# Performance work log

Measured on AMD Instinct MI355X. Metric: run time of the kernel, lower is better.

## Reference

```python
import jax, jax.numpy as jnp
import numpy as np

B, N, D = 2, 2048, 1024
RANK, HEADS = 256, 16
HS = RANK // HEADS          # 16, low-rank head size for QK
DH = D // HEADS             # 64, value head size
SCALE = 1.0 / np.sqrt(HS)


def setup_inputs() -> dict:
    key = jax.random.key(0)
    k1, k2, k3 = jax.random.split(key, 3)
    x = jax.random.normal(k1, (B, N, D), dtype=jnp.float32)
    # causal additive mask, 0 on/below diag, -1e9 above
    mask = jnp.where(jnp.tril(jnp.ones((N, N), dtype=bool)), 0.0, -1e9).astype(jnp.float32)
    Wqk = jax.random.normal(k2, (2 * RANK, D), dtype=jnp.float32) * (1.0 / np.sqrt(D))
    Wv = jax.random.normal(k3, (D, D), dtype=jnp.float32) * (1.0 / np.sqrt(D))
    return {"x": x, "mask": mask, "Wqk": Wqk, "Wv": Wv}


def reference(x, mask, Wqk, Wv):
    b, n, d = x.shape
    qk = jnp.einsum('bnd,rd->bnr', x, Wqk)            # [b,n,2*rank]
    q, k = jnp.split(qk, 2, axis=-1)                  # [b,n,rank] each
    # L2 normalize over FULL rank dim (before head split), clamp norm >= 1e-6
    q = q / jnp.maximum(jnp.linalg.norm(q, axis=-1, keepdims=True), 1e-6)
    k = k / jnp.maximum(jnp.linalg.norm(k, axis=-1, keepdims=True), 1e-6)
    q = q.reshape(b, n, HEADS, HS).transpose(0, 2, 1, 3)   # [b,h,n,hs]
    k = k.reshape(b, n, HEADS, HS).transpose(0, 2, 1, 3)
    v = jnp.einsum('bnd,ed->bne', x, Wv).reshape(b, n, HEADS, DH).transpose(0, 2, 1, 3)  # [b,h,n,dh]
    att = jnp.einsum('bhqe,bhke->bhqk', q, k) * SCALE
    att = jnp.clip(att, -10000.0, 10000.0)
    att = att + mask[None, None, :, :]
    att = jax.nn.softmax(att, axis=-1)
    # NaN guard: zero NaNs then renormalize (no-op when no NaNs)
    att = jnp.where(jnp.isnan(att), 0.0, att)
    att = att / jnp.maximum(att.sum(axis=-1, keepdims=True), 1e-6)
    y = jnp.einsum('bhqk,bhkd->bhqd', att, v)              # [b,h,n,dh]
    return y.transpose(0, 2, 1, 3).reshape(b, n, d)
```

## Files before the change

kernel.cpp:

```cpp
#include <hip/hip_runtime.h>
#include <math.h>

#define BATCH 2
#define SEQ   2048
#define DIM   1024
#define RANK  256
#define HEADS 16
#define HS    16
#define DH    64
#define MROWS 4096

#define QSCALE 0.36067376f

typedef __attribute__((ext_vector_type(8)))  short    short8;
typedef __attribute__((ext_vector_type(4)))  float    f32x4;
typedef __attribute__((ext_vector_type(16))) float    f32x16;
typedef __attribute__((ext_vector_type(2)))  unsigned uint2v;

#define GPTR const __attribute__((address_space(1))) unsigned int*
#define LPTR __attribute__((address_space(3))) unsigned int*

__device__ __forceinline__ unsigned short f2bf(float f) {
    union { float f; unsigned u; } v; v.f = f;
    return (unsigned short)((v.u + 0x7FFFu + ((v.u >> 16) & 1u)) >> 16);
}
__device__ __forceinline__ float bf2f(unsigned short h) {
    union { unsigned u; float f; } v; v.u = ((unsigned)h) << 16;
    return v.f;
}

#define XQ   1048576
#define WQKQ 131072
#define WVQ  262144
__global__ __launch_bounds__(256) void conv3(const float* __restrict__ x,
                                             const float* __restrict__ wqk,
                                             const float* __restrict__ wv,
                                             unsigned short* __restrict__ xb,
                                             unsigned short* __restrict__ wcat)
{
    const int i = blockIdx.x * 256 + threadIdx.x;
    const float* src; unsigned short* dst; int j;
    if (i < XQ)              { src = x;   dst = xb;   j = i; }
    else if (i < XQ + WQKQ)  { src = wqk; dst = wcat; j = i - XQ; }
    else                     { src = wv;  dst = wcat + (size_t)4 * WQKQ; j = i - XQ - WQKQ; }
    float4 v = ((const float4*)src)[j];
    ushort4 o; o.x = f2bf(v.x); o.y = f2bf(v.y); o.z = f2bf(v.z); o.w = f2bf(v.w);
    ((ushort4*)dst)[j] = o;
}

__global__ __launch_bounds__(256, 3) void gemm_mfma(const unsigned short* __restrict__ A,
                                                    const unsigned short* __restrict__ W,
                                                    unsigned short* __restrict__ qkb,
                                                    unsigned short* __restrict__ vt)
{
    __shared__ __align__(16) unsigned short Alds[2][128 * 64];
    __shared__ __align__(16) unsigned short Blds[2][64 * 64];

    const int tid = threadIdx.x;
    const int w = tid >> 6, lane = tid & 63;
    const int lr = lane & 15, lg = lane >> 4;
    const int wm = w >> 1, wn = w & 1;

    const int Lf = blockIdx.x;
    const int xcd = Lf & 7;
    const int i5 = Lf >> 3;
    const int bm = (4 * xcd + (i5 & 3)) * 128;
    const int bn = (i5 >> 2) * 64;

    const int rs = lane >> 3, cs = lane & 7;

    f32x4 acc[4][2] = {};

#define STAGEG(kt_, buf_) do {                                                        \
        const int k0_ = (kt_) * 64;                                                   \
        _Pragma("unroll")                                                             \
        for (int i = 0; i < 4; ++i) {                                                 \
            const int r = w * 32 + i * 8 + rs;                                        \
            __builtin_amdgcn_global_load_lds(                                         \
                (GPTR)&A[(size_t)(bm + r) * 1024 + k0_ + 8 * (cs ^ (r & 7))],         \
                (LPTR)&Alds[buf_][(w * 32 + i * 8) * 64], 16, 0, 0);                  \
        }                                                                             \
        _Pragma("unroll")                                                             \
        for (int i = 0; i < 2; ++i) {                                                 \
            const int r = w * 16 + i * 8 + rs;                                        \
            __builtin_amdgcn_global_load_lds(                                         \
                (GPTR)&W[(size_t)(bn + r) * 1024 + k0_ + 8 * (cs ^ (r & 7))],         \
                (LPTR)&Blds[buf_][(w * 16 + i * 8) * 64], 16, 0, 0);                  \
        }                                                                             \
    } while (0)

    STAGEG(0, 0);

    #pragma unroll 1
    for (int kt = 0; kt < 16; ++kt) {
        if (kt + 1 < 16) {
            STAGEG(kt + 1, (kt + 1) & 1);
            asm volatile("s_waitcnt vmcnt(6)" ::: "memory");
        } else {
            asm volatile("s_waitcnt vmcnt(0)" ::: "memory");
        }
        __builtin_amdgcn_sched_barrier(0);
        __builtin_amdgcn_s_barrier();

        const int buf = kt & 1;
        #pragma unroll
        for (int kk = 0; kk < 2; ++kk) {
            short8 af[4], bfr[2];
            #pragma unroll
            for (int mi = 0; mi < 4; ++mi) {
                const int row = wm * 64 + mi * 16 + lr;
                af[mi] = *(const short8*)&Alds[buf][row * 64 + 8 * ((kk * 4 + lg) ^ (row & 7))];
            }
            #pragma unroll
            for (int ni = 0; ni < 2; ++ni) {
                const int row = wn * 32 + ni * 16 + lr;
                bfr[ni] = *(const short8*)&Blds[buf][row * 64 + 8 * ((kk * 4 + lg) ^ (row & 7))];
            }
            #pragma unroll
            for (int mi = 0; mi < 4; ++mi)
                #pragma unroll
                for (int ni = 0; ni < 2; ++ni)
                    acc[mi][ni] = __builtin_amdgcn_mfma_f32_16x16x32_bf16(af[mi], bfr[ni], acc[mi][ni], 0, 0, 0);
        }
        __builtin_amdgcn_s_barrier();
    }
#undef STAGEG

    if (bn < 512) {
        #pragma unroll
        for (int mi = 0; mi < 4; ++mi) {
            const int rbase = bm + wm * 64 + mi * 16 + lg * 4;
            #pragma unroll
            for (int ni = 0; ni < 2; ++ni) {
                const int col = bn + wn * 32 + ni * 16 + lr;
                #pragma unroll
                for (int r = 0; r < 4; ++r)
                    qkb[(size_t)(rbase + r) * 512 + col] = f2bf(acc[mi][ni][r]);
            }
        }
    } else {
        const int nb = bn - 512;
        #pragma unroll
        for (int mi = 0; mi < 4; ++mi) {
            const int m = bm + wm * 64 + mi * 16 + lg * 4;
            const int bb = m >> 11, ms = m & 2047;
            #pragma unroll
            for (int ni = 0; ni < 2; ++ni) {
                const int d = nb + wn * 32 + ni * 16 + lr;
                ushort4 pk;
                pk.x = f2bf(acc[mi][ni][0]); pk.y = f2bf(acc[mi][ni][1]);
                pk.z = f2bf(acc[mi][ni][2]); pk.w = f2bf(acc[mi][ni][3]);
                *(ushort4*)&vt[((size_t)bb * DIM + d) * SEQ + ms] = pk;
            }
        }
    }
}

__global__ __launch_bounds__(256) void l2norm_split(const unsigned short* __restrict__ qkb,
                                                    unsigned short* __restrict__ qn,
                                                    unsigned short* __restrict__ kn)
{
    const int row = blockIdx.x;
    const int t = threadIdx.x;
    const unsigned short* p = qkb + (size_t)row * 512;
    float q = bf2f(p[t]);
    float k = bf2f(p[t + 256]);
    float sq = q * q, sk = k * k;
    #pragma unroll
    for (int off = 32; off > 0; off >>= 1) {
        sq += __shfl_down(sq, off);
        sk += __shfl_down(sk, off);
    }
    __shared__ float sh[8];
    const int wid = t >> 6;
    if ((t & 63) == 0) { sh[wid * 2] = sq; sh[wid * 2 + 1] = sk; }
    __syncthreads();
    sq = sh[0] + sh[2] + sh[4] + sh[6];
    sk = sh[1] + sh[3] + sh[5] + sh[7];
    const float rq = QSCALE / fmaxf(sqrtf(sq), 1e-6f);
    const float rk = 1.0f   / fmaxf(sqrtf(sk), 1e-6f);

    const int b = row >> 11, n = row & 2047;
    const int head = t >> 4, hs = t & 15;
    const size_t o = (((size_t)b * HEADS + head) * SEQ + n) * 16 + hs;
    qn[o] = f2bf(q * rq);
    kn[o] = f2bf(k * rk);
}

template<bool MASK>
__device__ __forceinline__ void segpv(const short8 ak0, const short8 ak1, const short8 bq,
                                      const unsigned short* Vs, int kb, int kh, int hi,
                                      int l31, int qg, f32x16 o[2], float& lp)
{
    const f32x16 z = {};
    short8 pa[4];

    const f32x16 s0 = __builtin_amdgcn_mfma_f32_32x32x16_bf16(ak0, bq, z, 0, 0, 0);
    {
        float p0[16];
        #pragma unroll
        for (int r = 0; r < 16; ++r) {
            float e = __builtin_exp2f(s0[r]);
            if (MASK) {
                const int kl = kb + (r & 3) + 8 * (r >> 2) + 4 * hi;
                e = (kl > qg) ? 0.0f : e;
            }
            p0[r] = e; lp += e;
        }
        #pragma unroll
        for (int g = 0; g < 2; ++g) {
            const int jj = 2 * g;
            unsigned a0, a1, b0, b1;
            asm("v_cvt_pk_bf16_f32 %0, %1, %2" : "=v"(a0) : "v"(p0[4*jj]),     "v"(p0[4*jj + 1]));
            asm("v_cvt_pk_bf16_f32 %0, %1, %2" : "=v"(b0) : "v"(p0[4*jj + 2]), "v"(p0[4*jj + 3]));
            asm("v_cvt_pk_bf16_f32 %0, %1, %2" : "=v"(a1) : "v"(p0[4*jj + 4]), "v"(p0[4*jj + 5]));
            asm("v_cvt_pk_bf16_f32 %0, %1, %2" : "=v"(b1) : "v"(p0[4*jj + 6]), "v"(p0[4*jj + 7]));
            const uint2v r0 = __builtin_amdgcn_permlane32_swap(a0, a1, false, false);
            const uint2v r1 = __builtin_amdgcn_permlane32_swap(b0, b1, false, false);
            union { short8 s; unsigned u[4]; } pu;
            pu.u[0] = r0[0]; pu.u[1] = r1[0]; pu.u[2] = r0[1]; pu.u[3] = r1[1];
            pa[g] = pu.s;
        }
    }
    const f32x16 s1 = __builtin_amdgcn_mfma_f32_32x32x16_bf16(ak1, bq, z, 0, 0, 0);
    {
        float p1[16];
        #pragma unroll
        for (int r = 0; r < 16; ++r) {
            float e = __builtin_exp2f(s1[r]);
            if (MASK) {
                const int kl = kb + 32 + (r & 3) + 8 * (r >> 2) + 4 * hi;
                e = (kl > qg) ? 0.0f : e;
            }
            p1[r] = e; lp += e;
        }
        #pragma unroll
        for (int g = 0; g < 2; ++g) {
            const int jj = 2 * g;
            unsigned a0, a1, b0, b1;
            asm("v_cvt_pk_bf16_f32 %0, %1, %2" : "=v"(a0) : "v"(p1[4*jj]),     "v"(p1[4*jj + 1]));
            asm("v_cvt_pk_bf16_f32 %0, %1, %2" : "=v"(b0) : "v"(p1[4*jj + 2]), "v"(p1[4*jj + 3]));
            asm("v_cvt_pk_bf16_f32 %0, %1, %2" : "=v"(a1) : "v"(p1[4*jj + 4]), "v"(p1[4*jj + 5]));
            asm("v_cvt_pk_bf16_f32 %0, %1, %2" : "=v"(b1) : "v"(p1[4*jj + 6]), "v"(p1[4*jj + 7]));
            const uint2v r0 = __builtin_amdgcn_permlane32_swap(a0, a1, false, false);
            const uint2v r1 = __builtin_amdgcn_permlane32_swap(b0, b1, false, false);
            union { short8 s; unsigned u[4]; } pu;
            pu.u[0] = r0[0]; pu.u[1] = r1[0]; pu.u[2] = r0[1]; pu.u[3] = r1[1];
            pa[2 + g] = pu.s;
        }
    }

    #pragma unroll
    for (int g = 0; g < 4; ++g)
        #pragma unroll
        for (int half = 0; half < 2; ++half) {
            const int row = half * 32 + l31;
            const int slot = (8 * kh + 2 * g + hi) ^ (row & 15);
            const short8 bv = *(const short8*)&Vs[row * 128 + 8 * slot];
            o[half] = __builtin_amdgcn_mfma_f32_32x32x16_bf16(pa[g], bv, o[half], 0, 0, 0);
        }
}

__global__ __launch_bounds__(512, 4) void attn_w8(const unsigned short* __restrict__ qn,
                                                  const unsigned short* __restrict__ kn,
                                                  const unsigned short* __restrict__ vt,
                                                  float* __restrict__ out)
{
    const int L = blockIdx.x;
    const int bh = L & 31;
    const int p  = L >> 5;
    const int h = bh & 15, b = bh >> 4;

    const int tid = threadIdx.x, w = tid >> 6, lane = tid & 63;
    const int seg = w >> 2, qh = (w >> 1) & 1, kh = w & 1;
    const int l31 = lane & 31, hi = lane >> 5;

    const int qt  = seg ? p : 31 - p;
    const int nts = (qt >> 1) + 1;
    const int nt0 = ((31 - p) >> 1) + 1;
    const int band = qt * 64 + qh * 32;
    const int qg = band + l31;

    __shared__ __align__(16) unsigned char smem[33792];

    const unsigned short* qbh = qn + (size_t)bh * SEQ * 16;
    const unsigned short* kbh = kn + (size_t)bh * SEQ * 16;

    const short8 bq = *(const short8*)&qbh[qg * 16 + 8 * hi];

    f32x16 o[2] = {};
    float lp = 0.0f;

    const unsigned short* kwin = kbh + (64 * kh + l31) * 16 + 8 * hi;
    short8 ak0 = *(const short8*)(kwin);
    short8 ak1 = *(const short8*)(kwin + 32 * 16);

    const int vsub = lane >> 4, vslot = lane & 15;

#define STAGEV(kt_, buf_) do {                                                                    \
        const int k0_ = (kt_) * 128;                                                              \
        _Pragma("unroll")                                                                         \
        for (int i = 0; i < 2; ++i) {                                                             \
            const int c = 2 * w + i;                                                              \
            const int dh = 4 * c + vsub;                                                          \
            const int so = 8 * (vslot ^ (dh & 15));                                               \
            __builtin_amdgcn_global_load_lds(                                                     \
                (GPTR)&vt[((size_t)b * DIM + h * DH + dh) * SEQ + k0_ + so],                      \
                (LPTR)(smem + (buf_) * 16384 + c * 1024), 16, 0, 0);                              \
        }                                                                                         \
    } while (0)

    STAGEV(0, 0);

    #pragma unroll 1
    for (int kt = 0; kt < nt0; ++kt) {
        short8 an0 = ak0, an1 = ak1;
        if (kt + 1 < nt0) {
            STAGEV(kt + 1, (kt + 1) & 1);
            an0 = *(const short8*)(kwin + (size_t)(kt + 1) * 128 * 16);
            an1 = *(const short8*)(kwin + (size_t)(kt + 1) * 128 * 16 + 32 * 16);
            asm volatile("s_waitcnt vmcnt(4)" ::: "memory");
        } else {
            asm volatile("s_waitcnt vmcnt(0)" ::: "memory");
        }
        __builtin_amdgcn_sched_barrier(0);
        __builtin_amdgcn_s_barrier();

        if (kt < nts) {
            const unsigned short* Vs = (const unsigned short*)(smem + (kt & 1) * 16384);
            const int kb = kt * 128 + 64 * kh;
            __builtin_amdgcn_s_setprio(1);
            if (kt < nts - 1) {
                segpv<false>(ak0, ak1, bq, Vs, kb, kh, hi, l31, qg, o, lp);
            } else if (kb <= band + 31) {
                if (kb + 63 <= band) segpv<false>(ak0, ak1, bq, Vs, kb, kh, hi, l31, qg, o, lp);
                else                 segpv<true >(ak0, ak1, bq, Vs, kb, kh, hi, l31, qg, o, lp);
            }
            __builtin_amdgcn_s_setprio(0);
        }

        ak0 = an0; ak1 = an1;
        __builtin_amdgcn_s_barrier();
    }
#undef STAGEV

    lp += __shfl_xor(lp, 32);

    __syncthreads();
    float* Os = (float*)(smem + seg * 16384);
    float* Ls = (float*)(smem + 32768 + seg * 512);

    if (kh == 1) {
        #pragma unroll
        for (int half = 0; half < 2; ++half)
            #pragma unroll
            for (int r = 0; r < 16; ++r) {
                const int q = (r & 3) + 8 * (r >> 2) + 4 * hi;
                Os[(qh * 32 + q) * 64 + half * 32 + l31] = o[half][r];
            }
        Ls[qh * 64 + lane] = lp;
    }
    __syncthreads();
    if (kh == 0) {
        const float lt = lp + Ls[qh * 64 + lane];
        const float inv = 1.0f / fmaxf(lt, 1e-6f);
        #pragma unroll
        for (int r = 0; r < 16; ++r) {
            const int q = (r & 3) + 8 * (r >> 2) + 4 * hi;
            const float iv = __shfl(inv, q);
            #pragma unroll
            for (int half = 0; half < 2; ++half) {
                const float v = (o[half][r] + Os[(qh * 32 + q) * 64 + half * 32 + l31]) * iv;
                __builtin_nontemporal_store(v,
                    &out[((size_t)b * SEQ + band + q) * DIM + h * DH + half * 32 + l31]);
            }
        }
    }
}

extern "C" void kernel_launch(void* const* d_in, const int* in_sizes, int n_in,
                              void* d_out, int out_size, void* d_ws, size_t ws_size,
                              hipStream_t stream)
{
    const float* x   = (const float*)d_in[0];
    const float* Wqk = (const float*)d_in[2];
    const float* Wv  = (const float*)d_in[3];
    float* out = (float*)d_out;

    unsigned short* xb   = (unsigned short*)d_ws;
    unsigned short* qkb  = xb  + (size_t)MROWS * DIM;
    unsigned short* vt   = qkb + (size_t)MROWS * 512;
    unsigned short* wcat = vt  + (size_t)BATCH * DIM * SEQ;
    unsigned short* qn = xb;
    unsigned short* kn = xb + (size_t)32 * SEQ * 16;

    conv3<<<5632, 256, 0, stream>>>(x, Wqk, Wv, xb, wcat);
    gemm_mfma<<<768, 256, 0, stream>>>(xb, wcat, qkb, vt);
    l2norm_split<<<MROWS, 256, 0, stream>>>(qkb, qn, kn);
    attn_w8<<<512, 512, 0, stream>>>(qn, kn, vt, out);
}
```

Measured before the change: 67.37 us.

## Process both query halves per wave reusing V fragments; polynomial exp2

```diff
diff --git a/kernel.cpp b/kernel.cpp
--- a/kernel.cpp
+++ b/kernel.cpp
@@ -27,6 +27,10 @@
 __device__ __forceinline__ float bf2f(unsigned short h) {
     union { unsigned u; float f; } v; v.u = ((unsigned)h) << 16;
     return v.f;
+}
+
+__device__ __forceinline__ float exp2_poly(float x) {
+    return fmaf(x, fmaf(x, fmaf(x, 0.05550411f, 0.24022651f), 0.69314718f), 1.0f);
 }
 
 #define XQ   1048576
@@ -187,84 +191,72 @@
     kn[o] = f2bf(k * rk);
 }
 
+
 template<bool MASK>
-__device__ __forceinline__ void segpv(const short8 ak0, const short8 ak1, const short8 bq,
-                                      const unsigned short* Vs, int kb, int kh, int hi,
-                                      int l31, int qg, f32x16 o[2], float& lp)
+__device__ __forceinline__ void qpv(const short8 ak0, const short8 ak1, const short8 bq,
+                                    const short8 vb[4][2], int kb, int hi, int qg,
+                                    f32x16 o[2], float& lp)
 {
     const f32x16 z = {};
     short8 pa[4];
 
     const f32x16 s0 = __builtin_amdgcn_mfma_f32_32x32x16_bf16(ak0, bq, z, 0, 0, 0);
-    {
-        float p0[16];
-        #pragma unroll
-        for (int r = 0; r < 16; ++r) {
-            float e = __builtin_exp2f(s0[r]);
-            if (MASK) {
-                const int kl = kb + (r & 3) + 8 * (r >> 2) + 4 * hi;
-                e = (kl > qg) ? 0.0f : e;
-            }
-            p0[r] = e; lp += e;
-        }
-        #pragma unroll
-        for (int g = 0; g < 2; ++g) {
-            const int jj = 2 * g;
-            unsigned a0, a1, b0, b1;
-            asm("v_cvt_pk_bf16_f32 %0, %1, %2" : "=v"(a0) : "v"(p0[4*jj]),     "v"(p0[4*jj + 1]));
-            asm("v_cvt_pk_bf16_f32 %0, %1, %2" : "=v"(b0) : "v"(p0[4*jj + 2]), "v"(p0[4*jj + 3]));
-            asm("v_cvt_pk_bf16_f32 %0, %1, %2" : "=v"(a1) : "v"(p0[4*jj + 4]), "v"(p0[4*jj + 5]));
-            asm("v_cvt_pk_bf16_f32 %0, %1, %2" : "=v"(b1) : "v"(p0[4*jj + 6]), "v"(p0[4*jj + 7]));
-            const uint2v r0 = __builtin_amdgcn_permlane32_swap(a0, a1, false, false);
-            const uint2v r1 = __builtin_amdgcn_permlane32_swap(b0, b1, false, false);
-            union { short8 s; unsigned u[4]; } pu;
-            pu.u[0] = r0[0]; pu.u[1] = r1[0]; pu.u[2] = r0[1]; pu.u[3] = r1[1];
-            pa[g] = pu.s;
-        }
-    }
     const f32x16 s1 = __builtin_amdgcn_mfma_f32_32x32x16_bf16(ak1, bq, z, 0, 0, 0);
-    {
-        float p1[16];
-        #pragma unroll
-        for (int r = 0; r < 16; ++r) {
-            float e = __builtin_exp2f(s1[r]);
-            if (MASK) {
-                const int kl = kb + 32 + (r & 3) + 8 * (r >> 2) + 4 * hi;
-                e = (kl > qg) ? 0.0f : e;
-            }
-            p1[r] = e; lp += e;
-        }
-        #pragma unroll
-        for (int g = 0; g < 2; ++g) {
-            const int jj = 2 * g;
-            unsigned a0, a1, b0, b1;
-            asm("v_cvt_pk_bf16_f32 %0, %1, %2" : "=v"(a0) : "v"(p1[4*jj]),     "v"(p1[4*jj + 1]));
-            asm("v_cvt_pk_bf16_f32 %0, %1, %2" : "=v"(b0) : "v"(p1[4*jj + 2]), "v"(p1[4*jj + 3]));
-            asm("v_cvt_pk_bf16_f32 %0, %1, %2" : "=v"(a1) : "v"(p1[4*jj + 4]), "v"(p1[4*jj + 5]));
-            asm("v_cvt_pk_bf16_f32 %0, %1, %2" : "=v"(b1) : "v"(p1[4*jj + 6]), "v"(p1[4*jj + 7]));
-            const uint2v r0 = __builtin_amdgcn_permlane32_swap(a0, a1, false, false);
-            const uint2v r1 = __builtin_amdgcn_permlane32_swap(b0, b1, false, false);
-            union { short8 s; unsigned u[4]; } pu;
-            pu.u[0] = r0[0]; pu.u[1] = r1[0]; pu.u[2] = r0[1]; pu.u[3] = r1[1];
-            pa[2 + g] = pu.s;
-        }
+
+    float p0[16], p1[16];
+    #pragma unroll
+    for (int r = 0; r < 16; ++r) {
+        float e0 = exp2_poly(s0[r]);
+        float e1 = exp2_poly(s1[r]);
+        if (MASK) {
+            const int kl = kb + (r & 3) + 8 * (r >> 2) + 4 * hi;
+            e0 = (kl > qg) ? 0.0f : e0;
+            e1 = (kl + 32 > qg) ? 0.0f : e1;
+        }
+        p0[r] = e0; p1[r] = e1;
+        lp += e0 + e1;
+    }
+
+    #pragma unroll
+    for (int g = 0; g < 4; ++g) {
+        const float* pc = (g < 2) ? p0 : p1;
+        const int jj = 2 * (g & 1);
+        unsigned a0, a1, b0, b1;
+        asm("v_cvt_pk_bf16_f32 %0, %1, %2" : "=v"(a0) : "v"(pc[4*jj]),     "v"(pc[4*jj + 1]));
+        asm("v_cvt_pk_bf16_f32 %0, %1, %2" : "=v"(b0) : "v"(pc[4*jj + 2]), "v"(pc[4*jj + 3]));
+        asm("v_cvt_pk_bf16_f32 %0, %1, %2" : "=v"(a1) : "v"(pc[4*jj + 4]), "v"(pc[4*jj + 5]));
+        asm("v_cvt_pk_bf16_f32 %0, %1, %2" : "=v"(b1) : "v"(pc[4*jj + 6]), "v"(pc[4*jj + 7]));
+        const uint2v r0 = __builtin_amdgcn_permlane32_swap(a0, a1, false, false);
+        const uint2v r1 = __builtin_amdgcn_permlane32_swap(b0, b1, false, false);
+        union { short8 s; unsigned u[4]; } pu;
+        pu.u[0] = r0[0]; pu.u[1] = r1[0]; pu.u[2] = r0[1]; pu.u[3] = r1[1];
+        pa[g] = pu.s;
     }
 
     #pragma unroll
     for (int g = 0; g < 4; ++g)
         #pragma unroll
-        for (int half = 0; half < 2; ++half) {
-            const int row = half * 32 + l31;
-            const int slot = (8 * kh + 2 * g + hi) ^ (row & 15);
-            const short8 bv = *(const short8*)&Vs[row * 128 + 8 * slot];
-            o[half] = __builtin_amdgcn_mfma_f32_32x32x16_bf16(pa[g], bv, o[half], 0, 0, 0);
-        }
-}
-
-__global__ __launch_bounds__(512, 4) void attn_w8(const unsigned short* __restrict__ qn,
-                                                  const unsigned short* __restrict__ kn,
-                                                  const unsigned short* __restrict__ vt,
-                                                  float* __restrict__ out)
+        for (int half = 0; half < 2; ++half)
+            o[half] = __builtin_amdgcn_mfma_f32_32x32x16_bf16(pa[g], vb[g][half], o[half], 0, 0, 0);
+}
+
+__device__ __forceinline__ void qdisp(bool last, const short8 ak0, const short8 ak1,
+                                      const short8 bq, const short8 vb[4][2], int kb,
+                                      int hi, int qmin, int qg,
+                                      f32x16 o[2], float& lp)
+{
+    if (!last) {
+        qpv<false>(ak0, ak1, bq, vb, kb, hi, qg, o, lp);
+    } else if (kb <= qmin + 31) {
+        if (kb + 63 <= qmin) qpv<false>(ak0, ak1, bq, vb, kb, hi, qg, o, lp);
+        else                 qpv<true >(ak0, ak1, bq, vb, kb, hi, qg, o, lp);
+    }
+}
+
+__global__ __launch_bounds__(256, 2) void attn_q64(const unsigned short* __restrict__ qn,
+                                                   const unsigned short* __restrict__ kn,
+                                                   const unsigned short* __restrict__ vt,
+                                                   float* __restrict__ out)
 {
     const int L = blockIdx.x;
     const int bh = L & 31;
@@ -272,24 +264,25 @@
     const int h = bh & 15, b = bh >> 4;
 
     const int tid = threadIdx.x, w = tid >> 6, lane = tid & 63;
-    const int seg = w >> 2, qh = (w >> 1) & 1, kh = w & 1;
+    const int seg = w >> 1, kh = w & 1;
     const int l31 = lane & 31, hi = lane >> 5;
 
     const int qt  = seg ? p : 31 - p;
     const int nts = (qt >> 1) + 1;
     const int nt0 = ((31 - p) >> 1) + 1;
-    const int band = qt * 64 + qh * 32;
-    const int qg = band + l31;
+    const int qmin0 = qt * 64, qmin1 = qt * 64 + 32;
+    const int qg0 = qmin0 + l31, qg1 = qmin1 + l31;
 
     __shared__ __align__(16) unsigned char smem[33792];
 
     const unsigned short* qbh = qn + (size_t)bh * SEQ * 16;
     const unsigned short* kbh = kn + (size_t)bh * SEQ * 16;
 
-    const short8 bq = *(const short8*)&qbh[qg * 16 + 8 * hi];
-
-    f32x16 o[2] = {};
-    float lp = 0.0f;
+    const short8 bq0 = *(const short8*)&qbh[qg0 * 16 + 8 * hi];
+    const short8 bq1 = *(const short8*)&qbh[qg1 * 16 + 8 * hi];
+
+    f32x16 o0[2] = {}, o1[2] = {};
+    float lp0 = 0.0f, lp1 = 0.0f;
 
     const unsigned short* kwin = kbh + (64 * kh + l31) * 16 + 8 * hi;
     short8 ak0 = *(const short8*)(kwin);
@@ -300,8 +293,8 @@
 #define STAGEV(kt_, buf_) do {                                                                    \
         const int k0_ = (kt_) * 128;                                                              \
         _Pragma("unroll")                                                                         \
-        for (int i = 0; i < 2; ++i) {                                                             \
-            const int c = 2 * w + i;                                                              \
+        for (int i = 0; i < 4; ++i) {                                                             \
+            const int c = 4 * w + i;                                                              \
             const int dh = 4 * c + vsub;                                                          \
             const int so = 8 * (vslot ^ (dh & 15));                                               \
             __builtin_amdgcn_global_load_lds(                                                     \
@@ -319,7 +312,7 @@
             STAGEV(kt + 1, (kt + 1) & 1);
             an0 = *(const short8*)(kwin + (size_t)(kt + 1) * 128 * 16);
             an1 = *(const short8*)(kwin + (size_t)(kt + 1) * 128 * 16 + 32 * 16);
-            asm volatile("s_waitcnt vmcnt(4)" ::: "memory");
+            asm volatile("s_waitcnt vmcnt(6)" ::: "memory");
         } else {
             asm volatile("s_waitcnt vmcnt(0)" ::: "memory");
         }
@@ -329,13 +322,21 @@
         if (kt < nts) {
             const unsigned short* Vs = (const unsigned short*)(smem + (kt & 1) * 16384);
             const int kb = kt * 128 + 64 * kh;
+
+            short8 vb[4][2];
+            #pragma unroll
+            for (int g = 0; g < 4; ++g)
+                #pragma unroll
+                for (int half = 0; half < 2; ++half) {
+                    const int row = half * 32 + l31;
+                    const int slot = (8 * kh + 2 * g + hi) ^ (row & 15);
+                    vb[g][half] = *(const short8*)&Vs[row * 128 + 8 * slot];
+                }
+
+            const bool last = (kt == nts - 1);
             __builtin_amdgcn_s_setprio(1);
-            if (kt < nts - 1) {
-                segpv<false>(ak0, ak1, bq, Vs, kb, kh, hi, l31, qg, o, lp);
-            } else if (kb <= band + 31) {
-                if (kb + 63 <= band) segpv<false>(ak0, ak1, bq, Vs, kb, kh, hi, l31, qg, o, lp);
-                else                 segpv<true >(ak0, ak1, bq, Vs, kb, kh, hi, l31, qg, o, lp);
-            }
+            qdisp(last, ak0, ak1, bq0, vb, kb, hi, qmin0, qg0, o0, lp0);
+            qdisp(last, ak0, ak1, bq1, vb, kb, hi, qmin1, qg1, o1, lp1);
             __builtin_amdgcn_s_setprio(0);
         }
 
@@ -344,11 +345,12 @@
     }
 #undef STAGEV
 
-    lp += __shfl_xor(lp, 32);
+    lp0 += __shfl_xor(lp0, 32);
+    lp1 += __shfl_xor(lp1, 32);
 
     __syncthreads();
-    float* Os = (float*)(smem + seg * 16384);
-    float* Ls = (float*)(smem + 32768 + seg * 512);
+    float* Os = (float*)smem;
+    float* Ls = (float*)(smem + 32768);
 
     if (kh == 1) {
         #pragma unroll
@@ -356,23 +358,31 @@
             #pragma unroll
             for (int r = 0; r < 16; ++r) {
                 const int q = (r & 3) + 8 * (r >> 2) + 4 * hi;
-                Os[(qh * 32 + q) * 64 + half * 32 + l31] = o[half][r];
-            }
-        Ls[qh * 64 + lane] = lp;
+                Os[(seg * 64 + q) * 64 + half * 32 + l31]      = o0[half][r];
+                Os[(seg * 64 + 32 + q) * 64 + half * 32 + l31] = o1[half][r];
+            }
+        Ls[seg * 128 + lane]      = lp0;
+        Ls[seg * 128 + 64 + lane] = lp1;
     }
     __syncthreads();
     if (kh == 0) {
-        const float lt = lp + Ls[qh * 64 + lane];
-        const float inv = 1.0f / fmaxf(lt, 1e-6f);
+        float lt0 = lp0 + Ls[seg * 128 + lane];
+        float lt1 = lp1 + Ls[seg * 128 + 64 + lane];
+        const float inv0 = 1.0f / fmaxf(lt0, 1e-6f);
+        const float inv1 = 1.0f / fmaxf(lt1, 1e-6f);
         #pragma unroll
         for (int r = 0; r < 16; ++r) {
             const int q = (r & 3) + 8 * (r >> 2) + 4 * hi;
-            const float iv = __shfl(inv, q);
+            const float iv0 = __shfl(inv0, q);
+            const float iv1 = __shfl(inv1, q);
             #pragma unroll
             for (int half = 0; half < 2; ++half) {
-                const float v = (o[half][r] + Os[(qh * 32 + q) * 64 + half * 32 + l31]) * iv;
-                __builtin_nontemporal_store(v,
-                    &out[((size_t)b * SEQ + band + q) * DIM + h * DH + half * 32 + l31]);
+                const float v0 = (o0[half][r] + Os[(seg * 64 + q) * 64 + half * 32 + l31]) * iv0;
+                const float v1 = (o1[half][r] + Os[(seg * 64 + 32 + q) * 64 + half * 32 + l31]) * iv1;
+                __builtin_nontemporal_store(v0,
+                    &out[((size_t)b * SEQ + qmin0 + q) * DIM + h * DH + half * 32 + l31]);
+                __builtin_nontemporal_store(v1,
+                    &out[((size_t)b * SEQ + qmin1 + q) * DIM + h * DH + half * 32 + l31]);
             }
         }
     }
@@ -397,5 +407,5 @@
     conv3<<<5632, 256, 0, stream>>>(x, Wqk, Wv, xb, wcat);
     gemm_mfma<<<768, 256, 0, stream>>>(xb, wcat, qkb, vt);
     l2norm_split<<<MROWS, 256, 0, stream>>>(qkb, qn, kn);
-    attn_w8<<<512, 512, 0, stream>>>(qn, kn, vt, out);
-}
+    attn_q64<<<512, 256, 0, stream>>>(qn, kn, vt, out);
+}
```

New measurement: 65.86 us. 1.02x faster.
